# Optimization experiments

Measured on AMD Instinct MI355X. Metric: run time of the kernel, lower is better.

The kernel has to match this reference:

```python
import jax, jax.numpy as jnp
import numpy as np

B, C, N = 2, 128, 784  # batch, channels, spatial tokens (28x28)
TEMPERATURE = 11.313708498984761  # sqrt(C)


def setup_inputs() -> dict:
    key = jax.random.key(0)
    kq, kk, kv = jax.random.split(key, 3)
    q = jax.random.normal(kq, (B, C, N), dtype=jnp.float32)
    k = jax.random.normal(kk, (B, C, N), dtype=jnp.float32)
    v = jax.random.normal(kv, (B, C, N), dtype=jnp.float32)
    return {"q": q, "k": k, "v": v}


def reference(q, k, v):
    # dist_func == 'l1' branch of ScaledDotProductAttention (eval mode, dropout=0)
    qs = q / TEMPERATURE                                   # [B, C, Nq]
    # torch: q.unsqueeze(2).repeat -> [B,C,Nk,Nq]; k.unsqueeze(3).repeat -> [B,C,Nk,Nq]
    # broadcast instead of repeat; mean over channel dim 1
    diff = jnp.abs(qs[:, :, None, :] - k[:, :, :, None])   # [B, C, Nk, Nq]
    attn = jnp.mean(diff, axis=1)                          # [B, Nk, Nq]
    attn = jax.nn.softmax(attn, axis=-1)                   # softmax over Nq (last dim)
    # torch.bmm(v, attn.permute(0,2,1)): out[b,c,k] = sum_q v[b,c,q] * attn[b,k,q]
    out = jnp.einsum("bcq,bkq->bck", v, attn)              # [B, C, Nk]
    return (out, attn)
```

## Files before the change

### kernel.cpp

```cpp
#include <hip/hip_runtime.h>
#include <math.h>

constexpr int kB = 2;
constexpr int kC = 128;
constexpr int kN = 784;
constexpr float kInvT = 1.0f / 11.313708498984761f;
constexpr float kInvC = 1.0f / 128.0f;

constexpr size_t kOutElems  = (size_t)kB * kC * kN;
constexpr size_t kAttnElems = (size_t)kB * kN * kN;

__device__ inline float wave_max(float v) {
#pragma unroll
    for (int o = 32; o > 0; o >>= 1) v = fmaxf(v, __shfl_xor(v, o, 64));
    return v;
}
__device__ inline float wave_sum(float v) {
#pragma unroll
    for (int o = 32; o > 0; o >>= 1) v += __shfl_xor(v, o, 64);
    return v;
}

constexpr int TK = 64;
constexpr int TQ = 64;
constexpr int NKT = (kN + TK - 1) / TK;
constexpr int NQT = (kN + TQ - 1) / TQ;
constexpr int CSP = 2;
constexpr int CH = kC / CSP;
constexpr int DSTR = 68;

template <bool USE_WS>
__global__ __launch_bounds__(256) void dist_kernel(const float* __restrict__ qg,
                                                   const float* __restrict__ kg,
                                                   float* __restrict__ D0,
                                                   float* __restrict__ D1) {
    int bid = blockIdx.x;
    const int qt = bid % NQT; bid /= NQT;
    const int kt = bid % NKT; bid /= NKT;
    const int ch = bid & 1;   bid >>= 1;
    const int b  = bid;
    const int k0 = kt * TK;
    const int q0 = qt * TQ;
    const int t  = threadIdx.x;

    __shared__ float ks[CH][DSTR];
    __shared__ float qs[CH][DSTR];

    const float* kb = kg + ((size_t)b * kC + ch * CH) * kN;
    const float* qb = qg + ((size_t)b * kC + ch * CH) * kN;

#pragma unroll
    for (int i = t; i < CH * 16; i += 256) {
        const int c  = i >> 4;
        const int x4 = (i & 15) << 2;
        *reinterpret_cast<float4*>(&ks[c][x4]) =
            *reinterpret_cast<const float4*>(kb + (size_t)c * kN + min(k0 + x4, kN - 4));
        float4 qv = *reinterpret_cast<const float4*>(qb + (size_t)c * kN + min(q0 + x4, kN - 4));
        qv.x *= kInvT; qv.y *= kInvT; qv.z *= kInvT; qv.w *= kInvT;
        *reinterpret_cast<float4*>(&qs[c][x4]) = qv;
    }
    __syncthreads();

    const int qx = (t & 15) << 2;
    const int kx = (t >> 4) << 2;

    float acc[4][4];
#pragma unroll
    for (int i = 0; i < 4; ++i)
#pragma unroll
        for (int j = 0; j < 4; ++j) acc[i][j] = 0.0f;

#pragma unroll 4
    for (int c = 0; c < CH; ++c) {
        const float4 kv = *reinterpret_cast<const float4*>(&ks[c][kx]);
        const float4 qv = *reinterpret_cast<const float4*>(&qs[c][qx]);
        const float kf[4] = {kv.x, kv.y, kv.z, kv.w};
        const float qf[4] = {qv.x, qv.y, qv.z, qv.w};
#pragma unroll
        for (int i = 0; i < 4; ++i)
#pragma unroll
            for (int j = 0; j < 4; ++j)
                acc[i][j] += fabsf(qf[j] - kf[i]);
    }

    const int qcol = q0 + qx;
    if (qcol < kN) {
        float* dst = (USE_WS && ch) ? D1 : D0;
#pragma unroll
        for (int i = 0; i < 4; ++i) {
            const int krow = k0 + kx + i;
            if (krow < kN) {
                const size_t off = ((size_t)b * kN + krow) * kN + qcol;
                if (USE_WS) {
                    *reinterpret_cast<float4*>(dst + off) =
                        make_float4(acc[i][0], acc[i][1], acc[i][2], acc[i][3]);
                } else {
                    atomicAdd(&D0[off + 0], acc[i][0]);
                    atomicAdd(&D0[off + 1], acc[i][1]);
                    atomicAdd(&D0[off + 2], acc[i][2]);
                    atomicAdd(&D0[off + 3], acc[i][3]);
                }
            }
        }
    }
}

template <bool SUM2>
__global__ __launch_bounds__(256) void softmax_kernel(float* __restrict__ A,
                                                      const float* __restrict__ W) {
    const size_t row = (size_t)blockIdx.x * kN;
    float4* A4 = reinterpret_cast<float4*>(A + row);
    const float4* W4 = reinterpret_cast<const float4*>(W + row);
    const int t = threadIdx.x;
    const int lane = t & 63, wid = t >> 6;
    const bool act = t < (kN / 4);
    __shared__ float xred[4];

    float4 x = make_float4(-1e30f, -1e30f, -1e30f, -1e30f);
    if (act) {
        x = A4[t];
        if (SUM2) {
            const float4 w = W4[t];
            x.x += w.x; x.y += w.y; x.z += w.z; x.w += w.w;
        }
    }

    float m = fmaxf(fmaxf(x.x, x.y), fmaxf(x.z, x.w));
    m = wave_max(m);
    if (lane == 0) xred[wid] = m;
    __syncthreads();
    m = fmaxf(fmaxf(xred[0], xred[1]), fmaxf(xred[2], xred[3]));
    __syncthreads();

    float4 p;
    p.x = __expf((x.x - m) * kInvC);
    p.y = __expf((x.y - m) * kInvC);
    p.z = __expf((x.z - m) * kInvC);
    p.w = __expf((x.w - m) * kInvC);
    float lsum = p.x + p.y + p.z + p.w;
    lsum = wave_sum(lsum);
    if (lane == 0) xred[wid] = lsum;
    __syncthreads();
    const float inv = 1.0f / (xred[0] + xred[1] + xred[2] + xred[3]);
    if (act) {
        p.x *= inv; p.y *= inv; p.z *= inv; p.w *= inv;
        A4[t] = p;
    }
}

constexpr int BKT = 64;
constexpr int NKT2 = (kN + BKT - 1) / BKT;
constexpr int QSP = 14;
constexpr int QPB = kN / QSP;
constexpr int QCH = 28;
constexpr int BSTR = 68;

template <bool ATOMIC>
__global__ __launch_bounds__(256) void bmm_stage1(const float* __restrict__ vg,
                                                  const float* __restrict__ attn,
                                                  float* __restrict__ P) {
    int bid = blockIdx.x;
    const int qs = bid % QSP;   bid /= QSP;
    const int kt = bid % NKT2;  bid /= NKT2;
    const int ct = bid & 1;     bid >>= 1;
    const int b  = bid;
    const int k0 = kt * BKT;
    const int c0 = ct * 64;
    const int qb0 = qs * QPB;
    const int t  = threadIdx.x;

    __shared__ float vT[QCH][BSTR];
    __shared__ float aT[QCH][BSTR];

    const int cc = t >> 2;
    const int j1 = t & 3;
    const int j2 = j1 + 4;
    const int c0l = (t >> 4) << 2;
    const int k0l = (t & 15) << 2;

    float acc[4][4];
#pragma unroll
    for (int i = 0; i < 4; ++i)
#pragma unroll
        for (int j = 0; j < 4; ++j) acc[i][j] = 0.0f;

    const float* vb = vg + ((size_t)b * kC + c0) * kN;
    const float* ab = attn + (size_t)b * kN * kN;
    const int krow_st = min(k0 + cc, kN - 1);

    for (int qc = 0; qc < QPB; qc += QCH) {
        const int q0 = qb0 + qc;
        const float4 vv1 = *reinterpret_cast<const float4*>(vb + (size_t)cc * kN + q0 + 4 * j1);
        const float4 av1 = *reinterpret_cast<const float4*>(ab + (size_t)krow_st * kN + q0 + 4 * j1);
        float4 vv2, av2;
        const bool has2 = (j2 < 7);
        if (has2) {
            vv2 = *reinterpret_cast<const float4*>(vb + (size_t)cc * kN + q0 + 4 * j2);
            av2 = *reinterpret_cast<const float4*>(ab + (size_t)krow_st * kN + q0 + 4 * j2);
        }
        __syncthreads();
        {
            const int r1 = 4 * j1;
            vT[r1 + 0][cc] = vv1.x; vT[r1 + 1][cc] = vv1.y;
            vT[r1 + 2][cc] = vv1.z; vT[r1 + 3][cc] = vv1.w;
            aT[r1 + 0][cc] = av1.x; aT[r1 + 1][cc] = av1.y;
            aT[r1 + 2][cc] = av1.z; aT[r1 + 3][cc] = av1.w;
            if (has2) {
                const int r2 = 4 * j2;
                vT[r2 + 0][cc] = vv2.x; vT[r2 + 1][cc] = vv2.y;
                vT[r2 + 2][cc] = vv2.z; vT[r2 + 3][cc] = vv2.w;
                aT[r2 + 0][cc] = av2.x; aT[r2 + 1][cc] = av2.y;
                aT[r2 + 2][cc] = av2.z; aT[r2 + 3][cc] = av2.w;
            }
        }
        __syncthreads();

#pragma unroll
        for (int qq = 0; qq < QCH; ++qq) {
            const float4 vf4 = *reinterpret_cast<const float4*>(&vT[qq][c0l]);
            const float4 af4 = *reinterpret_cast<const float4*>(&aT[qq][k0l]);
            const float vf[4] = {vf4.x, vf4.y, vf4.z, vf4.w};
            const float af[4] = {af4.x, af4.y, af4.z, af4.w};
#pragma unroll
            for (int i = 0; i < 4; ++i)
#pragma unroll
                for (int j = 0; j < 4; ++j) acc[i][j] += vf[i] * af[j];
        }
    }

    if (ATOMIC) {
#pragma unroll
        for (int i = 0; i < 4; ++i) {
            const int c = c0 + c0l + i;
#pragma unroll
            for (int j = 0; j < 4; ++j) {
                const int krow = k0 + k0l + j;
                if (krow < kN)
                    atomicAdd(&P[((size_t)b * kC + c) * kN + krow], acc[i][j]);
            }
        }
    } else if (k0 + k0l < kN) {
#pragma unroll
        for (int i = 0; i < 4; ++i) {
            const int c = c0 + c0l + i;
            *reinterpret_cast<float4*>(
                P + (((size_t)qs * kB + b) * kC + c) * kN + k0 + k0l) =
                make_float4(acc[i][0], acc[i][1], acc[i][2], acc[i][3]);
        }
    }
}

__global__ __launch_bounds__(256) void reduce_kernel(const float* __restrict__ P,
                                                     float* __restrict__ out) {
    const int idx = blockIdx.x * 256 + threadIdx.x;
    const float4* p = reinterpret_cast<const float4*>(P) + idx;
    float4 s = p[0];
#pragma unroll
    for (int qs = 1; qs < QSP; ++qs) {
        const float4 v = p[(size_t)qs * (kOutElems / 4)];
        s.x += v.x; s.y += v.y; s.z += v.z; s.w += v.w;
    }
    reinterpret_cast<float4*>(out)[idx] = s;
}

extern "C" void kernel_launch(void* const* d_in, const int* in_sizes, int n_in,
                              void* d_out, int out_size, void* d_ws, size_t ws_size,
                              hipStream_t stream) {
    const float* q = (const float*)d_in[0];
    const float* k = (const float*)d_in[1];
    const float* v = (const float*)d_in[2];

    float* out  = (float*)d_out;
    float* attn = out + kOutElems;
    float* P    = (float*)d_ws;
    float* D1   = P + (size_t)QSP * kOutElems;

    const size_t need = ((size_t)QSP * kOutElems + kAttnElems) * sizeof(float);

    if (ws_size >= need) {
        dist_kernel<true><<<kB * CSP * NKT * NQT, 256, 0, stream>>>(q, k, attn, D1);
        softmax_kernel<true><<<kB * kN, 256, 0, stream>>>(attn, D1);
        bmm_stage1<false><<<kB * 2 * NKT2 * QSP, 256, 0, stream>>>(v, attn, P);
        reduce_kernel<<<(int)(kOutElems / 4 / 256), 256, 0, stream>>>(P, out);
    } else {
        hipMemsetAsync(attn, 0, kAttnElems * sizeof(float), stream);
        hipMemsetAsync(out, 0, kOutElems * sizeof(float), stream);
        dist_kernel<false><<<kB * CSP * NKT * NQT, 256, 0, stream>>>(q, k, attn, nullptr);
        softmax_kernel<false><<<kB * kN, 256, 0, stream>>>(attn, attn);
        bmm_stage1<true><<<kB * 2 * NKT2 * QSP, 256, 0, stream>>>(v, attn, out);
    }
}
```

Measured before the change: 93.14 us.

## Fuse four stages into persistent kernel with global atomic grid barriers

```diff
diff --git a/kernel.cpp b/kernel.cpp
--- a/kernel.cpp
+++ b/kernel.cpp
@@ -10,6 +10,21 @@
 constexpr size_t kOutElems  = (size_t)kB * kC * kN;
 constexpr size_t kAttnElems = (size_t)kB * kN * kN;
 
+constexpr int GRID = 768;
+
+constexpr int TK = 64, TQ = 64;
+constexpr int NKT = 13, NQT = 13;
+constexpr int CSP = 2, CH = 64;
+constexpr int DSTR = 68;
+constexpr int NDIST = kB * CSP * NKT * NQT;
+
+constexpr int BKT = 64, NKT2 = 13;
+constexpr int QSP = 14, QPB = 56, QCH = 28;
+constexpr int BSTR = 68;
+constexpr int NBMM = kB * 2 * NKT2 * QSP;
+
+constexpr int NROWS = kB * kN;
+
 __device__ inline float wave_max(float v) {
 #pragma unroll
     for (int o = 32; o > 0; o >>= 1) v = fmaxf(v, __shfl_xor(v, o, 64));
@@ -21,38 +36,249 @@
     return v;
 }
 
-constexpr int TK = 64;
-constexpr int TQ = 64;
-constexpr int NKT = (kN + TK - 1) / TK;
-constexpr int NQT = (kN + TQ - 1) / TQ;
-constexpr int CSP = 2;
-constexpr int CH = kC / CSP;
-constexpr int DSTR = 68;
-
-template <bool USE_WS>
-__global__ __launch_bounds__(256) void dist_kernel(const float* __restrict__ qg,
-                                                   const float* __restrict__ kg,
-                                                   float* __restrict__ D0,
-                                                   float* __restrict__ D1) {
+__device__ inline void gbarrier(unsigned* ctr, unsigned target) {
+    __syncthreads();
+    if (threadIdx.x == 0) {
+        __hip_atomic_fetch_add(ctr, 1u, __ATOMIC_ACQ_REL, __HIP_MEMORY_SCOPE_AGENT);
+        long spin = 0;
+        while (__hip_atomic_load(ctr, __ATOMIC_ACQUIRE, __HIP_MEMORY_SCOPE_AGENT) < target) {
+            __builtin_amdgcn_s_sleep(8);
+            if (++spin > (1L << 20)) break;
+        }
+    }
+    __syncthreads();
+}
+
+__global__ __launch_bounds__(256, 3) void mega_kernel(const float* __restrict__ qg,
+                                                      const float* __restrict__ kg,
+                                                      const float* __restrict__ vg,
+                                                      float* __restrict__ out,
+                                                      float* __restrict__ attn,
+                                                      float* __restrict__ P,
+                                                      float* __restrict__ D1,
+                                                      unsigned* __restrict__ bar) {
+    const int t = threadIdx.x;
+
+    __shared__ union {
+        struct { float ks[CH][DSTR]; float qs[CH][DSTR]; } d;
+        struct { float vT[QCH][BSTR]; float aT[QCH][BSTR]; } m;
+    } sh;
+    __shared__ float xred[4];
+
+    for (int tile = blockIdx.x; tile < NDIST; tile += GRID) {
+        int bid = tile;
+        const int qt = bid % NQT; bid /= NQT;
+        const int kt = bid % NKT; bid /= NKT;
+        const int ch = bid & 1;   bid >>= 1;
+        const int b  = bid;
+        const int k0 = kt * TK;
+        const int q0 = qt * TQ;
+
+        const float* kb = kg + ((size_t)b * kC + ch * CH) * kN;
+        const float* qb = qg + ((size_t)b * kC + ch * CH) * kN;
+
+#pragma unroll
+        for (int i = t; i < CH * 16; i += 256) {
+            const int c  = i >> 4;
+            const int x4 = (i & 15) << 2;
+            *reinterpret_cast<float4*>(&sh.d.ks[c][x4]) =
+                *reinterpret_cast<const float4*>(kb + (size_t)c * kN + min(k0 + x4, kN - 4));
+            float4 qv = *reinterpret_cast<const float4*>(qb + (size_t)c * kN + min(q0 + x4, kN - 4));
+            qv.x *= kInvT; qv.y *= kInvT; qv.z *= kInvT; qv.w *= kInvT;
+            *reinterpret_cast<float4*>(&sh.d.qs[c][x4]) = qv;
+        }
+        __syncthreads();
+
+        const int qx = (t & 15) << 2;
+        const int kx = (t >> 4) << 2;
+
+        float acc[4][4];
+#pragma unroll
+        for (int i = 0; i < 4; ++i)
+#pragma unroll
+            for (int j = 0; j < 4; ++j) acc[i][j] = 0.0f;
+
+#pragma unroll 4
+        for (int c = 0; c < CH; ++c) {
+            const float4 kv = *reinterpret_cast<const float4*>(&sh.d.ks[c][kx]);
+            const float4 qv = *reinterpret_cast<const float4*>(&sh.d.qs[c][qx]);
+            const float kf[4] = {kv.x, kv.y, kv.z, kv.w};
+            const float qf[4] = {qv.x, qv.y, qv.z, qv.w};
+#pragma unroll
+            for (int i = 0; i < 4; ++i)
+#pragma unroll
+                for (int j = 0; j < 4; ++j)
+                    acc[i][j] += fabsf(qf[j] - kf[i]);
+        }
+
+        const int qcol = q0 + qx;
+        if (qcol < kN) {
+            float* dst = ch ? D1 : attn;
+#pragma unroll
+            for (int i = 0; i < 4; ++i) {
+                const int krow = k0 + kx + i;
+                if (krow < kN) {
+                    *reinterpret_cast<float4*>(&dst[((size_t)b * kN + krow) * kN + qcol]) =
+                        make_float4(acc[i][0], acc[i][1], acc[i][2], acc[i][3]);
+                }
+            }
+        }
+        __syncthreads();
+    }
+
+    gbarrier(bar, GRID);
+
+    {
+        const int lane = t & 63, wid = t >> 6;
+        const bool act = t < (kN / 4);
+        for (int r = blockIdx.x; r < NROWS; r += GRID) {
+            const size_t row = (size_t)r * kN;
+            float4* A4 = reinterpret_cast<float4*>(attn + row);
+            const float4* W4 = reinterpret_cast<const float4*>(D1 + row);
+
+            __syncthreads();
+
+            float4 x = make_float4(-1e30f, -1e30f, -1e30f, -1e30f);
+            if (act) {
+                x = A4[t];
+                const float4 w = W4[t];
+                x.x += w.x; x.y += w.y; x.z += w.z; x.w += w.w;
+            }
+
+            float m = fmaxf(fmaxf(x.x, x.y), fmaxf(x.z, x.w));
+            m = wave_max(m);
+            if (lane == 0) xred[wid] = m;
+            __syncthreads();
+            m = fmaxf(fmaxf(xred[0], xred[1]), fmaxf(xred[2], xred[3]));
+            __syncthreads();
+
+            float4 p;
+            p.x = __expf((x.x - m) * kInvC);
+            p.y = __expf((x.y - m) * kInvC);
+            p.z = __expf((x.z - m) * kInvC);
+            p.w = __expf((x.w - m) * kInvC);
+            float lsum = p.x + p.y + p.z + p.w;
+            lsum = wave_sum(lsum);
+            if (lane == 0) xred[wid] = lsum;
+            __syncthreads();
+            const float inv = 1.0f / (xred[0] + xred[1] + xred[2] + xred[3]);
+            if (act) {
+                p.x *= inv; p.y *= inv; p.z *= inv; p.w *= inv;
+                A4[t] = p;
+            }
+        }
+    }
+
+    gbarrier(bar, 2u * GRID);
+
+    for (int tile = blockIdx.x; tile < NBMM; tile += GRID) {
+        int bid = tile;
+        const int qs = bid % QSP;   bid /= QSP;
+        const int kt = bid % NKT2;  bid /= NKT2;
+        const int ct = bid & 1;     bid >>= 1;
+        const int b  = bid;
+        const int k0 = kt * BKT;
+        const int c0 = ct * 64;
+        const int qb0 = qs * QPB;
+
+        const int cc = t >> 2;
+        const int j1 = t & 3;
+        const int j2 = j1 + 4;
+        const int c0l = (t >> 4) << 2;
+        const int k0l = (t & 15) << 2;
+
+        float acc[4][4];
+#pragma unroll
+        for (int i = 0; i < 4; ++i)
+#pragma unroll
+            for (int j = 0; j < 4; ++j) acc[i][j] = 0.0f;
+
+        const float* vb = vg + ((size_t)b * kC + c0) * kN;
+        const float* ab = attn + (size_t)b * kN * kN;
+        const int krow_st = min(k0 + cc, kN - 1);
+
+        for (int qc = 0; qc < QPB; qc += QCH) {
+            const int q0 = qb0 + qc;
+            const float4 vv1 = *reinterpret_cast<const float4*>(vb + (size_t)cc * kN + q0 + 4 * j1);
+            const float4 av1 = *reinterpret_cast<const float4*>(ab + (size_t)krow_st * kN + q0 + 4 * j1);
+            float4 vv2, av2;
+            const bool has2 = (j2 < 7);
+            if (has2) {
+                vv2 = *reinterpret_cast<const float4*>(vb + (size_t)cc * kN + q0 + 4 * j2);
+                av2 = *reinterpret_cast<const float4*>(ab + (size_t)krow_st * kN + q0 + 4 * j2);
+            }
+            __syncthreads();
+            {
+                const int r1 = 4 * j1;
+                sh.m.vT[r1 + 0][cc] = vv1.x; sh.m.vT[r1 + 1][cc] = vv1.y;
+                sh.m.vT[r1 + 2][cc] = vv1.z; sh.m.vT[r1 + 3][cc] = vv1.w;
+                sh.m.aT[r1 + 0][cc] = av1.x; sh.m.aT[r1 + 1][cc] = av1.y;
+                sh.m.aT[r1 + 2][cc] = av1.z; sh.m.aT[r1 + 3][cc] = av1.w;
+                if (has2) {
+                    const int r2 = 4 * j2;
+                    sh.m.vT[r2 + 0][cc] = vv2.x; sh.m.vT[r2 + 1][cc] = vv2.y;
+                    sh.m.vT[r2 + 2][cc] = vv2.z; sh.m.vT[r2 + 3][cc] = vv2.w;
+                    sh.m.aT[r2 + 0][cc] = av2.x; sh.m.aT[r2 + 1][cc] = av2.y;
+                    sh.m.aT[r2 + 2][cc] = av2.z; sh.m.aT[r2 + 3][cc] = av2.w;
+                }
+            }
+            __syncthreads();
+
+#pragma unroll
+            for (int qq = 0; qq < QCH; ++qq) {
+                const float4 vf4 = *reinterpret_cast<const float4*>(&sh.m.vT[qq][c0l]);
+                const float4 af4 = *reinterpret_cast<const float4*>(&sh.m.aT[qq][k0l]);
+                const float vf[4] = {vf4.x, vf4.y, vf4.z, vf4.w};
+                const float af[4] = {af4.x, af4.y, af4.z, af4.w};
+#pragma unroll
+                for (int i = 0; i < 4; ++i)
+#pragma unroll
+                    for (int j = 0; j < 4; ++j) acc[i][j] += vf[i] * af[j];
+            }
+        }
+
+        if (k0 + k0l < kN) {
+#pragma unroll
+            for (int i = 0; i < 4; ++i) {
+                const int c = c0 + c0l + i;
+                *reinterpret_cast<float4*>(
+                    P + (((size_t)qs * kB + b) * kC + c) * kN + k0 + k0l) =
+                    make_float4(acc[i][0], acc[i][1], acc[i][2], acc[i][3]);
+            }
+        }
+        __syncthreads();
+    }
+
+    gbarrier(bar, 3u * GRID);
+
+    for (int idx = (int)blockIdx.x * 256 + t; idx < (int)(kOutElems / 4); idx += GRID * 256) {
+        const float4* p = reinterpret_cast<const float4*>(P) + idx;
+        float4 s = p[0];
+#pragma unroll
+        for (int qs = 1; qs < QSP; ++qs) {
+            const float4 v = p[(size_t)qs * (kOutElems / 4)];
+            s.x += v.x; s.y += v.y; s.z += v.z; s.w += v.w;
+        }
+        reinterpret_cast<float4*>(out)[idx] = s;
+    }
+}
+
+__global__ __launch_bounds__(256) void dist_fb(const float* __restrict__ qg,
+                                               const float* __restrict__ kg,
+                                               float* __restrict__ D0) {
     int bid = blockIdx.x;
     const int qt = bid % NQT; bid /= NQT;
     const int kt = bid % NKT; bid /= NKT;
     const int ch = bid & 1;   bid >>= 1;
     const int b  = bid;
-    const int k0 = kt * TK;
-    const int q0 = qt * TQ;
-    const int t  = threadIdx.x;
-
+    const int k0 = kt * TK, q0 = qt * TQ;
+    const int t = threadIdx.x;
     __shared__ float ks[CH][DSTR];
     __shared__ float qs[CH][DSTR];
-
     const float* kb = kg + ((size_t)b * kC + ch * CH) * kN;
     const float* qb = qg + ((size_t)b * kC + ch * CH) * kN;
-
-#pragma unroll
     for (int i = t; i < CH * 16; i += 256) {
-        const int c  = i >> 4;
-        const int x4 = (i & 15) << 2;
+        const int c = i >> 4, x4 = (i & 15) << 2;
         *reinterpret_cast<float4*>(&ks[c][x4]) =
             *reinterpret_cast<const float4*>(kb + (size_t)c * kN + min(k0 + x4, kN - 4));
         float4 qv = *reinterpret_cast<const float4*>(qb + (size_t)c * kN + min(q0 + x4, kN - 4));
@@ -60,134 +286,76 @@
         *reinterpret_cast<float4*>(&qs[c][x4]) = qv;
     }
     __syncthreads();
-
-    const int qx = (t & 15) << 2;
-    const int kx = (t >> 4) << 2;
-
+    const int qx = (t & 15) << 2, kx = (t >> 4) << 2;
     float acc[4][4];
-#pragma unroll
     for (int i = 0; i < 4; ++i)
-#pragma unroll
         for (int j = 0; j < 4; ++j) acc[i][j] = 0.0f;
-
-#pragma unroll 4
     for (int c = 0; c < CH; ++c) {
         const float4 kv = *reinterpret_cast<const float4*>(&ks[c][kx]);
         const float4 qv = *reinterpret_cast<const float4*>(&qs[c][qx]);
         const float kf[4] = {kv.x, kv.y, kv.z, kv.w};
         const float qf[4] = {qv.x, qv.y, qv.z, qv.w};
-#pragma unroll
         for (int i = 0; i < 4; ++i)
-#pragma unroll
-            for (int j = 0; j < 4; ++j)
-                acc[i][j] += fabsf(qf[j] - kf[i]);
-    }
-
+            for (int j = 0; j < 4; ++j) acc[i][j] += fabsf(qf[j] - kf[i]);
+    }
     const int qcol = q0 + qx;
-    if (qcol < kN) {
-        float* dst = (USE_WS && ch) ? D1 : D0;
-#pragma unroll
+    if (qcol < kN)
         for (int i = 0; i < 4; ++i) {
             const int krow = k0 + kx + i;
             if (krow < kN) {
                 const size_t off = ((size_t)b * kN + krow) * kN + qcol;
-                if (USE_WS) {
-                    *reinterpret_cast<float4*>(dst + off) =
-                        make_float4(acc[i][0], acc[i][1], acc[i][2], acc[i][3]);
-                } else {
-                    atomicAdd(&D0[off + 0], acc[i][0]);
-                    atomicAdd(&D0[off + 1], acc[i][1]);
-                    atomicAdd(&D0[off + 2], acc[i][2]);
-                    atomicAdd(&D0[off + 3], acc[i][3]);
-                }
-            }
-        }
-    }
-}
-
-template <bool SUM2>
-__global__ __launch_bounds__(256) void softmax_kernel(float* __restrict__ A,
-                                                      const float* __restrict__ W) {
-    const size_t row = (size_t)blockIdx.x * kN;
-    float4* A4 = reinterpret_cast<float4*>(A + row);
-    const float4* W4 = reinterpret_cast<const float4*>(W + row);
-    const int t = threadIdx.x;
-    const int lane = t & 63, wid = t >> 6;
+                atomicAdd(&D0[off + 0], acc[i][0]);
+                atomicAdd(&D0[off + 1], acc[i][1]);
+                atomicAdd(&D0[off + 2], acc[i][2]);
+                atomicAdd(&D0[off + 3], acc[i][3]);
+            }
+        }
+}
+
+__global__ __launch_bounds__(256) void softmax_fb(float* __restrict__ A) {
+    float4* A4 = reinterpret_cast<float4*>(A + (size_t)blockIdx.x * kN);
+    const int t = threadIdx.x, lane = t & 63, wid = t >> 6;
     const bool act = t < (kN / 4);
     __shared__ float xred[4];
-
     float4 x = make_float4(-1e30f, -1e30f, -1e30f, -1e30f);
-    if (act) {
-        x = A4[t];
-        if (SUM2) {
-            const float4 w = W4[t];
-            x.x += w.x; x.y += w.y; x.z += w.z; x.w += w.w;
-        }
-    }
-
+    if (act) x = A4[t];
     float m = fmaxf(fmaxf(x.x, x.y), fmaxf(x.z, x.w));
     m = wave_max(m);
     if (lane == 0) xred[wid] = m;
     __syncthreads();
     m = fmaxf(fmaxf(xred[0], xred[1]), fmaxf(xred[2], xred[3]));
     __syncthreads();
-
     float4 p;
-    p.x = __expf((x.x - m) * kInvC);
-    p.y = __expf((x.y - m) * kInvC);
-    p.z = __expf((x.z - m) * kInvC);
-    p.w = __expf((x.w - m) * kInvC);
-    float lsum = p.x + p.y + p.z + p.w;
-    lsum = wave_sum(lsum);
-    if (lane == 0) xred[wid] = lsum;
+    p.x = __expf((x.x - m) * kInvC); p.y = __expf((x.y - m) * kInvC);
+    p.z = __expf((x.z - m) * kInvC); p.w = __expf((x.w - m) * kInvC);
+    float ls = p.x + p.y + p.z + p.w;
+    ls = wave_sum(ls);
+    if (lane == 0) xred[wid] = ls;
     __syncthreads();
     const float inv = 1.0f / (xred[0] + xred[1] + xred[2] + xred[3]);
-    if (act) {
-        p.x *= inv; p.y *= inv; p.z *= inv; p.w *= inv;
-        A4[t] = p;
-    }
-}
-
-constexpr int BKT = 64;
-constexpr int NKT2 = (kN + BKT - 1) / BKT;
-constexpr int QSP = 14;
-constexpr int QPB = kN / QSP;
-constexpr int QCH = 28;
-constexpr int BSTR = 68;
-
-template <bool ATOMIC>
-__global__ __launch_bounds__(256) void bmm_stage1(const float* __restrict__ vg,
-                                                  const float* __restrict__ attn,
-                                                  float* __restrict__ P) {
+    if (act) { p.x *= inv; p.y *= inv; p.z *= inv; p.w *= inv; A4[t] = p; }
+}
+
+__global__ __launch_bounds__(256) void bmm_fb(const float* __restrict__ vg,
+                                              const float* __restrict__ attn,
+                                              float* __restrict__ out) {
     int bid = blockIdx.x;
     const int qs = bid % QSP;   bid /= QSP;
     const int kt = bid % NKT2;  bid /= NKT2;
     const int ct = bid & 1;     bid >>= 1;
     const int b  = bid;
-    const int k0 = kt * BKT;
-    const int c0 = ct * 64;
-    const int qb0 = qs * QPB;
-    const int t  = threadIdx.x;
-
+    const int k0 = kt * BKT, c0 = ct * 64, qb0 = qs * QPB;
+    const int t = threadIdx.x;
     __shared__ float vT[QCH][BSTR];
     __shared__ float aT[QCH][BSTR];
-
-    const int cc = t >> 2;
-    const int j1 = t & 3;
-    const int j2 = j1 + 4;
-    const int c0l = (t >> 4) << 2;
-    const int k0l = (t & 15) << 2;
-
+    const int cc = t >> 2, j1 = t & 3, j2 = j1 + 4;
+    const int c0l = (t >> 4) << 2, k0l = (t & 15) << 2;
     float acc[4][4];
-#pragma unroll
     for (int i = 0; i < 4; ++i)
-#pragma unroll
         for (int j = 0; j < 4; ++j) acc[i][j] = 0.0f;
-
     const float* vb = vg + ((size_t)b * kC + c0) * kN;
     const float* ab = attn + (size_t)b * kN * kN;
     const int krow_st = min(k0 + cc, kN - 1);
-
     for (int qc = 0; qc < QPB; qc += QCH) {
         const int q0 = qb0 + qc;
         const float4 vv1 = *reinterpret_cast<const float4*>(vb + (size_t)cc * kN + q0 + 4 * j1);
@@ -199,68 +367,36 @@
             av2 = *reinterpret_cast<const float4*>(ab + (size_t)krow_st * kN + q0 + 4 * j2);
         }
         __syncthreads();
-        {
-            const int r1 = 4 * j1;
-            vT[r1 + 0][cc] = vv1.x; vT[r1 + 1][cc] = vv1.y;
-            vT[r1 + 2][cc] = vv1.z; vT[r1 + 3][cc] = vv1.w;
-            aT[r1 + 0][cc] = av1.x; aT[r1 + 1][cc] = av1.y;
-            aT[r1 + 2][cc] = av1.z; aT[r1 + 3][cc] = av1.w;
-            if (has2) {
-                const int r2 = 4 * j2;
-                vT[r2 + 0][cc] = vv2.x; vT[r2 + 1][cc] = vv2.y;
-                vT[r2 + 2][cc] = vv2.z; vT[r2 + 3][cc] = vv2.w;
-                aT[r2 + 0][cc] = av2.x; aT[r2 + 1][cc] = av2.y;
-                aT[r2 + 2][cc] = av2.z; aT[r2 + 3][cc] = av2.w;
-            }
+        const int r1 = 4 * j1;
+        vT[r1 + 0][cc] = vv1.x; vT[r1 + 1][cc] = vv1.y;
+        vT[r1 + 2][cc] = vv1.z; vT[r1 + 3][cc] = vv1.w;
+        aT[r1 + 0][cc] = av1.x; aT[r1 + 1][cc] = av1.y;
+        aT[r1 + 2][cc] = av1.z; aT[r1 + 3][cc] = av1.w;
+        if (has2) {
+            const int r2 = 4 * j2;
+            vT[r2 + 0][cc] = vv2.x; vT[r2 + 1][cc] = vv2.y;
+            vT[r2 + 2][cc] = vv2.z; vT[r2 + 3][cc] = vv2.w;
+            aT[r2 + 0][cc] = av2.x; aT[r2 + 1][cc] = av2.y;
+            aT[r2 + 2][cc] = av2.z; aT[r2 + 3][cc] = av2.w;
         }
         __syncthreads();
-
-#pragma unroll
         for (int qq = 0; qq < QCH; ++qq) {
             const float4 vf4 = *reinterpret_cast<const float4*>(&vT[qq][c0l]);
             const float4 af4 = *reinterpret_cast<const float4*>(&aT[qq][k0l]);
             const float vf[4] = {vf4.x, vf4.y, vf4.z, vf4.w};
             const float af[4] = {af4.x, af4.y, af4.z, af4.w};
-#pragma unroll
             for (int i = 0; i < 4; ++i)
-#pragma unroll
                 for (int j = 0; j < 4; ++j) acc[i][j] += vf[i] * af[j];
         }
     }
-
-    if (ATOMIC) {
-#pragma unroll
-        for (int i = 0; i < 4; ++i) {
-            const int c = c0 + c0l + i;
-#pragma unroll
-            for (int j = 0; j < 4; ++j) {
-                const int krow = k0 + k0l + j;
-                if (krow < kN)
-                    atomicAdd(&P[((size_t)b * kC + c) * kN + krow], acc[i][j]);
-            }
-        }
-    } else if (k0 + k0l < kN) {
-#pragma unroll
-        for (int i = 0; i < 4; ++i) {
-            const int c = c0 + c0l + i;
-            *reinterpret_cast<float4*>(
-                P + (((size_t)qs * kB + b) * kC + c) * kN + k0 + k0l) =
-                make_float4(acc[i][0], acc[i][1], acc[i][2], acc[i][3]);
-        }
-    }
-}
-
-__global__ __launch_bounds__(256) void reduce_kernel(const float* __restrict__ P,
-                                                     float* __restrict__ out) {
-    const int idx = blockIdx.x * 256 + threadIdx.x;
-    const float4* p = reinterpret_cast<const float4*>(P) + idx;
-    float4 s = p[0];
-#pragma unroll
-    for (int qs = 1; qs < QSP; ++qs) {
-        const float4 v = p[(size_t)qs * (kOutElems / 4)];
-        s.x += v.x; s.y += v.y; s.z += v.z; s.w += v.w;
-    }
-    reinterpret_cast<float4*>(out)[idx] = s;
+    for (int i = 0; i < 4; ++i) {
+        const int c = c0 + c0l + i;
+        for (int j = 0; j < 4; ++j) {
+            const int krow = k0 + k0l + j;
+            if (krow < kN)
+                atomicAdd(&out[((size_t)b * kC + c) * kN + krow], acc[i][j]);
+        }
+    }
 }
 
 extern "C" void kernel_launch(void* const* d_in, const int* in_sizes, int n_in,
@@ -274,19 +410,18 @@
     float* attn = out + kOutElems;
     float* P    = (float*)d_ws;
     float* D1   = P + (size_t)QSP * kOutElems;
-
-    const size_t need = ((size_t)QSP * kOutElems + kAttnElems) * sizeof(float);
+    unsigned* bar = (unsigned*)(D1 + kAttnElems);
+
+    const size_t need = ((size_t)QSP * kOutElems + kAttnElems) * sizeof(float) + 64;
 
     if (ws_size >= need) {
-        dist_kernel<true><<<kB * CSP * NKT * NQT, 256, 0, stream>>>(q, k, attn, D1);
-        softmax_kernel<true><<<kB * kN, 256, 0, stream>>>(attn, D1);
-        bmm_stage1<false><<<kB * 2 * NKT2 * QSP, 256, 0, stream>>>(v, attn, P);
-        reduce_kernel<<<(int)(kOutElems / 4 / 256), 256, 0, stream>>>(P, out);
+        hipMemsetAsync(bar, 0, 16, stream);
+        mega_kernel<<<GRID, 256, 0, stream>>>(q, k, v, out, attn, P, D1, bar);
     } else {
         hipMemsetAsync(attn, 0, kAttnElems * sizeof(float), stream);
         hipMemsetAsync(out, 0, kOutElems * sizeof(float), stream);
-        dist_kernel<false><<<kB * CSP * NKT * NQT, 256, 0, stream>>>(q, k, attn, nullptr);
-        softmax_kernel<false><<<kB * kN, 256, 0, stream>>>(attn, attn);
-        bmm_stage1<true><<<kB * 2 * NKT2 * QSP, 256, 0, stream>>>(v, attn, out);
-    }
-}
+        dist_fb<<<kB * CSP * NKT * NQT, 256, 0, stream>>>(q, k, attn);
+        softmax_fb<<<NROWS, 256, 0, stream>>>(attn);
+        bmm_fb<<<NBMM, 256, 0, stream>>>(v, attn, out);
+    }
+}
```

Measured after the change: 282.8 us. 204% more time.

## Fuse exp into distance kernel and defer softmax normalization past bmm

Applied to the files above, without the earlier changes.

```diff
diff --git a/kernel.cpp b/kernel.cpp
--- a/kernel.cpp
+++ b/kernel.cpp
@@ -10,6 +10,20 @@
 constexpr size_t kOutElems  = (size_t)kB * kC * kN;
 constexpr size_t kAttnElems = (size_t)kB * kN * kN;
 
+constexpr int DK = 32, DQ = 64;
+constexpr int DNKT = 25, DNQT = 13;
+constexpr int NDISTE = kB * DNKT * DNQT;
+constexpr int KSTR = 36, QSTR = 68;
+
+constexpr int BKT = 64, NKT2 = 13;
+constexpr int QSP = 14, QPB = 56, QCH = 28;
+constexpr int BSTR = 68;
+constexpr int NBMM = kB * 2 * NKT2 * QSP;
+
+constexpr int NROWS = kB * kN;
+constexpr int NNORM = NROWS / 4;
+constexpr int NOUTB = (int)(kOutElems / 4 / 256);
+
 __device__ inline float wave_max(float v) {
 #pragma unroll
     for (int o = 32; o > 0; o >>= 1) v = fmaxf(v, __shfl_xor(v, o, 64));
@@ -21,40 +35,35 @@
     return v;
 }
 
-constexpr int TK = 64;
-constexpr int TQ = 64;
-constexpr int NKT = (kN + TK - 1) / TK;
-constexpr int NQT = (kN + TQ - 1) / TQ;
-constexpr int CSP = 2;
-constexpr int CH = kC / CSP;
-constexpr int DSTR = 68;
-
-template <bool USE_WS>
-__global__ __launch_bounds__(256) void dist_kernel(const float* __restrict__ qg,
-                                                   const float* __restrict__ kg,
-                                                   float* __restrict__ D0,
-                                                   float* __restrict__ D1) {
+__global__ __launch_bounds__(128) void dist_exp(const float* __restrict__ qg,
+                                                const float* __restrict__ kg,
+                                                float* __restrict__ attn,
+                                                float* __restrict__ lp) {
     int bid = blockIdx.x;
-    const int qt = bid % NQT; bid /= NQT;
-    const int kt = bid % NKT; bid /= NKT;
-    const int ch = bid & 1;   bid >>= 1;
+    const int qt = bid % DNQT; bid /= DNQT;
+    const int kt = bid % DNKT; bid /= DNKT;
     const int b  = bid;
-    const int k0 = kt * TK;
-    const int q0 = qt * TQ;
+    const int k0 = kt * DK;
+    const int q0 = qt * DQ;
     const int t  = threadIdx.x;
 
-    __shared__ float ks[CH][DSTR];
-    __shared__ float qs[CH][DSTR];
-
-    const float* kb = kg + ((size_t)b * kC + ch * CH) * kN;
-    const float* qb = qg + ((size_t)b * kC + ch * CH) * kN;
-
-#pragma unroll
-    for (int i = t; i < CH * 16; i += 256) {
+    __shared__ float ks[kC][KSTR];
+    __shared__ float qs[kC][QSTR];
+
+    const float* kb = kg + (size_t)b * kC * kN;
+    const float* qb = qg + (size_t)b * kC * kN;
+
+#pragma unroll
+    for (int i = t; i < kC * 8; i += 128) {
+        const int c  = i >> 3;
+        const int x4 = (i & 7) << 2;
+        *reinterpret_cast<float4*>(&ks[c][x4]) =
+            *reinterpret_cast<const float4*>(kb + (size_t)c * kN + min(k0 + x4, kN - 4));
+    }
+#pragma unroll
+    for (int i = t; i < kC * 16; i += 128) {
         const int c  = i >> 4;
         const int x4 = (i & 15) << 2;
-        *reinterpret_cast<float4*>(&ks[c][x4]) =
-            *reinterpret_cast<const float4*>(kb + (size_t)c * kN + min(k0 + x4, kN - 4));
         float4 qv = *reinterpret_cast<const float4*>(qb + (size_t)c * kN + min(q0 + x4, kN - 4));
         qv.x *= kInvT; qv.y *= kInvT; qv.z *= kInvT; qv.w *= kInvT;
         *reinterpret_cast<float4*>(&qs[c][x4]) = qv;
@@ -71,7 +80,7 @@
         for (int j = 0; j < 4; ++j) acc[i][j] = 0.0f;
 
 #pragma unroll 4
-    for (int c = 0; c < CH; ++c) {
+    for (int c = 0; c < kC; ++c) {
         const float4 kv = *reinterpret_cast<const float4*>(&ks[c][kx]);
         const float4 qv = *reinterpret_cast<const float4*>(&qs[c][qx]);
         const float kf[4] = {kv.x, kv.y, kv.z, kv.w};
@@ -83,77 +92,42 @@
                 acc[i][j] += fabsf(qf[j] - kf[i]);
     }
 
+#pragma unroll
+    for (int i = 0; i < 4; ++i)
+#pragma unroll
+        for (int j = 0; j < 4; ++j)
+            acc[i][j] = __expf(acc[i][j] * kInvC);
+
     const int qcol = q0 + qx;
-    if (qcol < kN) {
-        float* dst = (USE_WS && ch) ? D1 : D0;
+    const bool qvalid = qcol < kN;
+    if (qvalid) {
 #pragma unroll
         for (int i = 0; i < 4; ++i) {
             const int krow = k0 + kx + i;
             if (krow < kN) {
-                const size_t off = ((size_t)b * kN + krow) * kN + qcol;
-                if (USE_WS) {
-                    *reinterpret_cast<float4*>(dst + off) =
-                        make_float4(acc[i][0], acc[i][1], acc[i][2], acc[i][3]);
-                } else {
-                    atomicAdd(&D0[off + 0], acc[i][0]);
-                    atomicAdd(&D0[off + 1], acc[i][1]);
-                    atomicAdd(&D0[off + 2], acc[i][2]);
-                    atomicAdd(&D0[off + 3], acc[i][3]);
-                }
+                *reinterpret_cast<float4*>(&attn[((size_t)b * kN + krow) * kN + qcol]) =
+                    make_float4(acc[i][0], acc[i][1], acc[i][2], acc[i][3]);
             }
         }
     }
-}
-
-template <bool SUM2>
-__global__ __launch_bounds__(256) void softmax_kernel(float* __restrict__ A,
-                                                      const float* __restrict__ W) {
-    const size_t row = (size_t)blockIdx.x * kN;
-    float4* A4 = reinterpret_cast<float4*>(A + row);
-    const float4* W4 = reinterpret_cast<const float4*>(W + row);
-    const int t = threadIdx.x;
-    const int lane = t & 63, wid = t >> 6;
-    const bool act = t < (kN / 4);
-    __shared__ float xred[4];
-
-    float4 x = make_float4(-1e30f, -1e30f, -1e30f, -1e30f);
-    if (act) {
-        x = A4[t];
-        if (SUM2) {
-            const float4 w = W4[t];
-            x.x += w.x; x.y += w.y; x.z += w.z; x.w += w.w;
-        }
-    }
-
-    float m = fmaxf(fmaxf(x.x, x.y), fmaxf(x.z, x.w));
-    m = wave_max(m);
-    if (lane == 0) xred[wid] = m;
-    __syncthreads();
-    m = fmaxf(fmaxf(xred[0], xred[1]), fmaxf(xred[2], xred[3]));
-    __syncthreads();
-
-    float4 p;
-    p.x = __expf((x.x - m) * kInvC);
-    p.y = __expf((x.y - m) * kInvC);
-    p.z = __expf((x.z - m) * kInvC);
-    p.w = __expf((x.w - m) * kInvC);
-    float lsum = p.x + p.y + p.z + p.w;
-    lsum = wave_sum(lsum);
-    if (lane == 0) xred[wid] = lsum;
-    __syncthreads();
-    const float inv = 1.0f / (xred[0] + xred[1] + xred[2] + xred[3]);
-    if (act) {
-        p.x *= inv; p.y *= inv; p.z *= inv; p.w *= inv;
-        A4[t] = p;
-    }
-}
-
-constexpr int BKT = 64;
-constexpr int NKT2 = (kN + BKT - 1) / BKT;
-constexpr int QSP = 14;
-constexpr int QPB = kN / QSP;
-constexpr int QCH = 28;
-constexpr int BSTR = 68;
+
+    float psum[4];
+#pragma unroll
+    for (int i = 0; i < 4; ++i)
+        psum[i] = qvalid ? (acc[i][0] + acc[i][1] + acc[i][2] + acc[i][3]) : 0.0f;
+#pragma unroll
+    for (int m = 1; m < 16; m <<= 1) {
+#pragma unroll
+        for (int i = 0; i < 4; ++i)
+            psum[i] += __shfl_xor(psum[i], m, 64);
+    }
+    if ((t & 15) == 0) {
+        const int base = ((b * DNKT + kt) * DNQT + qt) * DK + kx;
+#pragma unroll
+        for (int i = 0; i < 4; ++i)
+            lp[base + i] = psum[i];
+    }
+}
 
 template <bool ATOMIC>
 __global__ __launch_bounds__(256) void bmm_stage1(const float* __restrict__ vg,
@@ -250,17 +224,129 @@
     }
 }
 
-__global__ __launch_bounds__(256) void reduce_kernel(const float* __restrict__ P,
-                                                     float* __restrict__ out) {
-    const int idx = blockIdx.x * 256 + threadIdx.x;
-    const float4* p = reinterpret_cast<const float4*>(P) + idx;
-    float4 s = p[0];
-#pragma unroll
-    for (int qs = 1; qs < QSP; ++qs) {
-        const float4 v = p[(size_t)qs * (kOutElems / 4)];
-        s.x += v.x; s.y += v.y; s.z += v.z; s.w += v.w;
-    }
-    reinterpret_cast<float4*>(out)[idx] = s;
+__global__ __launch_bounds__(256) void finalize(float* __restrict__ attn,
+                                                const float* __restrict__ P,
+                                                const float* __restrict__ lp,
+                                                float* __restrict__ out) {
+    const int t = threadIdx.x;
+    if ((int)blockIdx.x < NNORM) {
+        const int wid = t >> 6, lane = t & 63;
+        const int r = (int)blockIdx.x * 4 + wid;
+        const int b = r / kN, k = r % kN;
+        const int kt = k >> 5, kk = k & 31;
+        const int base = ((b * DNKT + kt) * DNQT) * DK + kk;
+        float l = 0.0f;
+#pragma unroll
+        for (int qt = 0; qt < DNQT; ++qt) l += lp[base + qt * DK];
+        const float inv = 1.0f / l;
+
+        float4* A4 = reinterpret_cast<float4*>(attn + (size_t)r * kN);
+        float4 x0 = A4[lane], x1 = A4[lane + 64], x2 = A4[lane + 128];
+        x0.x *= inv; x0.y *= inv; x0.z *= inv; x0.w *= inv;
+        x1.x *= inv; x1.y *= inv; x1.z *= inv; x1.w *= inv;
+        x2.x *= inv; x2.y *= inv; x2.z *= inv; x2.w *= inv;
+        A4[lane] = x0; A4[lane + 64] = x1; A4[lane + 128] = x2;
+        if (lane < 4) {
+            float4 x3 = A4[lane + 192];
+            x3.x *= inv; x3.y *= inv; x3.z *= inv; x3.w *= inv;
+            A4[lane + 192] = x3;
+        }
+    } else {
+        const int idx = ((int)blockIdx.x - NNORM) * 256 + t;
+        const int e0 = idx * 4;
+        const int k4 = e0 % kN;
+        const int row = e0 / kN;
+        const int b = row >> 7;
+        const int kt = k4 >> 5, kk = k4 & 31;
+        const int base = ((b * DNKT + kt) * DNQT) * DK + kk;
+        float4 l4 = make_float4(0.f, 0.f, 0.f, 0.f);
+#pragma unroll
+        for (int qt = 0; qt < DNQT; ++qt) {
+            const float4 v = *reinterpret_cast<const float4*>(&lp[base + qt * DK]);
+            l4.x += v.x; l4.y += v.y; l4.z += v.z; l4.w += v.w;
+        }
+        const float4* p = reinterpret_cast<const float4*>(P) + idx;
+        float4 s = p[0];
+#pragma unroll
+        for (int qs = 1; qs < QSP; ++qs) {
+            const float4 v = p[(size_t)qs * (kOutElems / 4)];
+            s.x += v.x; s.y += v.y; s.z += v.z; s.w += v.w;
+        }
+        s.x /= l4.x; s.y /= l4.y; s.z /= l4.z; s.w /= l4.w;
+        reinterpret_cast<float4*>(out)[idx] = s;
+    }
+}
+
+__global__ __launch_bounds__(256) void dist_fb(const float* __restrict__ qg,
+                                               const float* __restrict__ kg,
+                                               float* __restrict__ D0) {
+    int bid = blockIdx.x;
+    const int qt = bid % DNQT; bid /= DNQT;
+    const int kt = bid % DNKT; bid /= DNKT;
+    const int b  = bid;
+    const int k0 = kt * DK, q0 = qt * DQ;
+    const int t = threadIdx.x;
+    __shared__ float ks[kC][KSTR];
+    __shared__ float qs[kC][QSTR];
+    const float* kb = kg + (size_t)b * kC * kN;
+    const float* qb = qg + (size_t)b * kC * kN;
+    for (int i = t; i < kC * 8; i += 128) {
+        const int c = i >> 3, x4 = (i & 7) << 2;
+        *reinterpret_cast<float4*>(&ks[c][x4]) =
+            *reinterpret_cast<const float4*>(kb + (size_t)c * kN + min(k0 + x4, kN - 4));
+    }
+    for (int i = t; i < kC * 16; i += 128) {
+        const int c = i >> 4, x4 = (i & 15) << 2;
+        float4 qv = *reinterpret_cast<const float4*>(qb + (size_t)c * kN + min(q0 + x4, kN - 4));
+        qv.x *= kInvT; qv.y *= kInvT; qv.z *= kInvT; qv.w *= kInvT;
+        *reinterpret_cast<float4*>(&qs[c][x4]) = qv;
+    }
+    __syncthreads();
+    const int qx = (t & 15) << 2, kx = (t >> 4) << 2;
+    float acc[4][4];
+    for (int i = 0; i < 4; ++i)
+        for (int j = 0; j < 4; ++j) acc[i][j] = 0.0f;
+    for (int c = 0; c < kC; ++c) {
+        const float4 kv = *reinterpret_cast<const float4*>(&ks[c][kx]);
+        const float4 qv = *reinterpret_cast<const float4*>(&qs[c][qx]);
+        const float kf[4] = {kv.x, kv.y, kv.z, kv.w};
+        const float qf[4] = {qv.x, qv.y, qv.z, qv.w};
+        for (int i = 0; i < 4; ++i)
+            for (int j = 0; j < 4; ++j) acc[i][j] += fabsf(qf[j] - kf[i]);
+    }
+    const int qcol = q0 + qx;
+    if (qcol < kN)
+        for (int i = 0; i < 4; ++i) {
+            const int krow = k0 + kx + i;
+            if (krow < kN) {
+                *reinterpret_cast<float4*>(&D0[((size_t)b * kN + krow) * kN + qcol]) =
+                    make_float4(acc[i][0], acc[i][1], acc[i][2], acc[i][3]);
+            }
+        }
+}
+
+__global__ __launch_bounds__(256) void softmax_fb(float* __restrict__ A) {
+    float4* A4 = reinterpret_cast<float4*>(A + (size_t)blockIdx.x * kN);
+    const int t = threadIdx.x, lane = t & 63, wid = t >> 6;
+    const bool act = t < (kN / 4);
+    __shared__ float xred[4];
+    float4 x = make_float4(-1e30f, -1e30f, -1e30f, -1e30f);
+    if (act) x = A4[t];
+    float m = fmaxf(fmaxf(x.x, x.y), fmaxf(x.z, x.w));
+    m = wave_max(m);
+    if (lane == 0) xred[wid] = m;
+    __syncthreads();
+    m = fmaxf(fmaxf(xred[0], xred[1]), fmaxf(xred[2], xred[3]));
+    __syncthreads();
+    float4 p;
+    p.x = __expf((x.x - m) * kInvC); p.y = __expf((x.y - m) * kInvC);
+    p.z = __expf((x.z - m) * kInvC); p.w = __expf((x.w - m) * kInvC);
+    float ls = p.x + p.y + p.z + p.w;
+    ls = wave_sum(ls);
+    if (lane == 0) xred[wid] = ls;
+    __syncthreads();
+    const float inv = 1.0f / (xred[0] + xred[1] + xred[2] + xred[3]);
+    if (act) { p.x *= inv; p.y *= inv; p.z *= inv; p.w *= inv; A4[t] = p; }
 }
 
 extern "C" void kernel_launch(void* const* d_in, const int* in_sizes, int n_in,
@@ -273,20 +359,18 @@
     float* out  = (float*)d_out;
     float* attn = out + kOutElems;
     float* P    = (float*)d_ws;
-    float* D1   = P + (size_t)QSP * kOutElems;
-
-    const size_t need = ((size_t)QSP * kOutElems + kAttnElems) * sizeof(float);
+    float* lp   = P + (size_t)QSP * kOutElems;
+
+    const size_t need = ((size_t)QSP * kOutElems + (size_t)NDISTE * DK) * sizeof(float);
 
     if (ws_size >= need) {
-        dist_kernel<true><<<kB * CSP * NKT * NQT, 256, 0, stream>>>(q, k, attn, D1);
-        softmax_kernel<true><<<kB * kN, 256, 0, stream>>>(attn, D1);
-        bmm_stage1<false><<<kB * 2 * NKT2 * QSP, 256, 0, stream>>>(v, attn, P);
-        reduce_kernel<<<(int)(kOutElems / 4 / 256), 256, 0, stream>>>(P, out);
+        dist_exp<<<NDISTE, 128, 0, stream>>>(q, k, attn, lp);
+        bmm_stage1<false><<<NBMM, 256, 0, stream>>>(v, attn, P);
+        finalize<<<NNORM + NOUTB, 256, 0, stream>>>(attn, P, lp, out);
     } else {
-        hipMemsetAsync(attn, 0, kAttnElems * sizeof(float), stream);
         hipMemsetAsync(out, 0, kOutElems * sizeof(float), stream);
-        dist_kernel<false><<<kB * CSP * NKT * NQT, 256, 0, stream>>>(q, k, attn, nullptr);
-        softmax_kernel<false><<<kB * kN, 256, 0, stream>>>(attn, attn);
-        bmm_stage1<true><<<kB * 2 * NKT2 * QSP, 256, 0, stream>>>(v, attn, out);
-    }
-}
+        dist_fb<<<NDISTE, 128, 0, stream>>>(q, k, attn);
+        softmax_fb<<<NROWS, 256, 0, stream>>>(attn);
+        bmm_stage1<true><<<NBMM, 256, 0, stream>>>(v, attn, out);
+    }
+}
```

New measurement: 99.11 us. +6.4%, slower.
